# Performance work log

Measured on AMD Instinct MI355X. Metric: run time of the kernel, lower is better.

Reference implementation:

```python
import jax, jax.numpy as jnp
import numpy as np

V = 32000   # vocab_size
H = 256     # num_hiddens
B = 32      # batch
T = 128     # seq_len


def setup_inputs() -> dict:
    key = jax.random.key(0)
    ks = jax.random.split(key, 10)
    s = 0.05  # keep pre-activations in a sane range
    return {
        "X": jax.random.randint(ks[0], (B, T), 0, V),
        "H0": jnp.zeros((B, H), jnp.float32),
        "Wz": (jax.random.normal(ks[1], (H, V + H)) * s).astype(jnp.float32),
        "bz": (jax.random.normal(ks[2], (H,)) * s).astype(jnp.float32),
        "Wr": (jax.random.normal(ks[3], (H, V + H)) * s).astype(jnp.float32),
        "br": (jax.random.normal(ks[4], (H,)) * s).astype(jnp.float32),
        "Wh": (jax.random.normal(ks[5], (H, V + H)) * s).astype(jnp.float32),
        "bh": (jax.random.normal(ks[6], (H,)) * s).astype(jnp.float32),
        "Wo": (jax.random.normal(ks[7], (V, H)) * s).astype(jnp.float32),
        "bo": (jax.random.normal(ks[8], (V,)) * s).astype(jnp.float32),
    }


def reference(X, H0, Wz, bz, Wr, br, Wh, bh, Wo, bo):
    # nn.Linear(cat(one_hot(x), h)) == gather of the vocab-columns + h @ Wh.T.
    # one_hot(x) @ W[:, :V].T  ==  W[:, :V].T[x]  (row gather), same math, no dense one-hot GEMM.
    vocab = Wo.shape[0]
    Wz_x, Wz_h = Wz[:, :vocab], Wz[:, vocab:]
    Wr_x, Wr_h = Wr[:, :vocab], Wr[:, vocab:]
    Wh_x, Wh_h = Wh[:, :vocab], Wh[:, vocab:]

    Xt = X.T                 # [T, B] -- matches X.T in torch forward
    gz = Wz_x.T[Xt]          # [T, B, H]
    gr = Wr_x.T[Xt]          # [T, B, H]
    gh = Wh_x.T[Xt]          # [T, B, H]

    def step(Hs, g):
        gz_t, gr_t, gh_t = g
        z = jax.nn.sigmoid(gz_t + Hs @ Wz_h.T + bz)
        r = jax.nn.sigmoid(gr_t + Hs @ Wr_h.T + br)
        h = jnp.tanh(gh_t + (r * Hs) @ Wh_h.T + bh)
        Hn = z * h + (1.0 - z) * Hs
        Y = Hn @ Wo.T + bo   # [B, V]
        return Hn, Y

    Hf, Ys = jax.lax.scan(step, H0, (gz, gr, gh))  # Ys: [T, B, V]
    # torch.cat(outputs, dim=0) stacks time-major -> [T*B, V]
    return Ys.reshape(-1, vocab), Hf
```

## Files before the change

### kernel.cpp

```cpp
#include <hip/hip_runtime.h>
#include <hip/hip_fp16.h>
#include <stdint.h>

#define VV 32000
#define HH 256
#define BB 32
#define TT 128
#define VH 32256

typedef _Float16 f16;
typedef _Float16 f16x2 __attribute__((ext_vector_type(2)));
typedef _Float16 f16x8 __attribute__((ext_vector_type(8)));
typedef float f32x4 __attribute__((ext_vector_type(4)));

static __device__ __forceinline__ float dot2f(uint32_t w, uint32_t h, float acc){
  f16x2 a = __builtin_bit_cast(f16x2, w);
  f16x2 b = __builtin_bit_cast(f16x2, h);
#if __has_builtin(__builtin_amdgcn_fdot2)
  return __builtin_amdgcn_fdot2(a, b, acc, false);
#else
  acc = fmaf((float)a[0], (float)b[0], acc);
  acc = fmaf((float)a[1], (float)b[1], acc);
  return acc;
#endif
}

__global__ void k_gather(const int* __restrict__ X,
                         const float* __restrict__ Wz, const float* __restrict__ bz,
                         const float* __restrict__ Wr, const float* __restrict__ br,
                         const float* __restrict__ Wh, const float* __restrict__ bh,
                         float* __restrict__ g_buf){
  int tb = blockIdx.x;
  int t = tb >> 5, b = tb & 31;
  int tok = X[b*TT + t];
  int o = threadIdx.x;
  g_buf[(size_t)tb*768 + o]       = Wz[(size_t)o*VH + tok] + bz[o];
  g_buf[(size_t)tb*768 + 256 + o] = Wr[(size_t)o*VH + tok] + br[o];
  g_buf[(size_t)tb*768 + 512 + o] = Wh[(size_t)o*VH + tok] + bh[o];
}

__global__ void k_pack(const float* __restrict__ Wz, const float* __restrict__ Wr,
                       const float* __restrict__ Wh, uint32_t* __restrict__ Wpack){
  int idx = blockIdx.x*256 + threadIdx.x;
  if (idx >= 512*192) return;
  int t = idx / 192, rem = idx - t*192;
  int ol = rem >> 4, p = rem & 15;
  int ko = t & 7, no = t >> 3;
  int k = ko*32 + p*2;
  const float* W; int row;
  if (ol < 8){ int o = no*8 + ol; if (o < 256){ W = Wz; row = o; } else { W = Wr; row = o - 256; } }
  else { W = Wh; row = no*4 + (ol - 8); }
  float a = W[(size_t)row*VH + VV + k];
  float c = W[(size_t)row*VH + VV + k + 1];
  f16x2 v; v[0] = (f16)a; v[1] = (f16)c;
  Wpack[idx] = __builtin_bit_cast(uint32_t, v);
}

__global__ __launch_bounds__(512)
__attribute__((amdgpu_waves_per_eu(2, 2)))
void k_recur(const float* __restrict__ H0,
             const uint32_t* __restrict__ Wpack,
             const float* __restrict__ g_buf,
             f16* __restrict__ Hn16,
             float* __restrict__ hf_out){
  __shared__ __align__(16) uint32_t hs16[128];
  __shared__ __align__(16) f16 rHs16[256];
  __shared__ float hs32[256];
  __shared__ float z_s[256];

  const int b = blockIdx.x;
  const int tid = threadIdx.x;
  const int ko = tid & 7, no = tid >> 3;

  uint32_t w[12][16];
  {
    const uint4* src = (const uint4*)(Wpack + (size_t)tid*192);
    #pragma unroll
    for (int j=0;j<48;j++){
      uint4 v = src[j];
      int f = j*4;
      w[(f+0)>>4][(f+0)&15] = v.x;
      w[(f+1)>>4][(f+1)&15] = v.y;
      w[(f+2)>>4][(f+2)&15] = v.z;
      w[(f+3)>>4][(f+3)&15] = v.w;
    }
  }

  if (tid < 256) hs32[tid] = H0[b*HH + tid];
  __syncthreads();
  if (tid < 128){
    f16x2 v; v[0] = (f16)hs32[2*tid]; v[1] = (f16)hs32[2*tid+1];
    hs16[tid] = __builtin_bit_cast(uint32_t, v);
  }
  __syncthreads();

  const int gi1 = no*8 + ko;
  const int gi2 = 512 + no*4 + (ko & 3);
  float g1 = g_buf[(size_t)b*768 + gi1];
  float g2 = g_buf[(size_t)b*768 + gi2];
  float g1n = 0.f, g2n = 0.f;

  for (int t = 0; t < TT; t++){
    if (t < TT-1){
      const float* gn = g_buf + (size_t)((t+1)*BB + b)*768;
      g1n = gn[gi1];
      g2n = gn[gi2];
    }

    uint32_t hp[16];
    {
      const uint2* hsp = (const uint2*)hs16;
      #pragma unroll
      for (int j=0;j<8;j++){ uint2 v = hsp[ko*8 + j]; hp[2*j] = v.x; hp[2*j+1] = v.y; }
    }
    float acc[8];
    #pragma unroll
    for (int ol=0;ol<8;ol++) acc[ol] = 0.f;
    #pragma unroll
    for (int p=0;p<16;p++)
      #pragma unroll
      for (int ol=0;ol<8;ol++)
        acc[ol] = dot2f(w[ol][p], hp[p], acc[ol]);
    #pragma unroll
    for (int ol=0;ol<8;ol++){
      float v2 = acc[ol];
      v2 += __shfl_xor(v2, 1);
      v2 += __shfl_xor(v2, 2);
      v2 += __shfl_xor(v2, 4);
      acc[ol] = v2;
    }
    {
      float sel = acc[0];
      #pragma unroll
      for (int ol=1;ol<8;ol++) sel = (ko == ol) ? acc[ol] : sel;
      float pre = sel + g1;
      float s = 1.f / (1.f + __expf(-pre));
      int o = no*8 + ko;
      if (no < 32){
        z_s[o] = s;
      } else {
        int op = o - 256;
        rHs16[op] = (f16)(s * hs32[op]);
      }
    }
    __syncthreads();

    uint32_t rp[16];
    {
      const uint2* rpp = (const uint2*)rHs16;
      #pragma unroll
      for (int j=0;j<8;j++){ uint2 v = rpp[ko*8 + j]; rp[2*j] = v.x; rp[2*j+1] = v.y; }
    }
    float a2[4];
    #pragma unroll
    for (int oi=0;oi<4;oi++) a2[oi] = 0.f;
    #pragma unroll
    for (int p=0;p<16;p++)
      #pragma unroll
      for (int oi=0;oi<4;oi++)
        a2[oi] = dot2f(w[8+oi][p], rp[p], a2[oi]);
    #pragma unroll
    for (int oi=0;oi<4;oi++){
      float v2 = a2[oi];
      v2 += __shfl_xor(v2, 1);
      v2 += __shfl_xor(v2, 2);
      v2 += __shfl_xor(v2, 4);
      a2[oi] = v2;
    }
    if (ko < 4){
      float sel = a2[0];
      #pragma unroll
      for (int oi=1;oi<4;oi++) sel = (ko == oi) ? a2[oi] : sel;
      int o = no*4 + ko;
      float pre = sel + g2;
      float ax = fabsf(pre);
      float e = __expf(2.f*ax);
      float th = 1.f - 2.f/(e + 1.f);
      th = copysignf(th, pre);
      float z = z_s[o];
      float hn = z*th + (1.f - z)*hs32[o];
      hs32[o] = hn;
      ((f16*)hs16)[o] = (f16)hn;
      Hn16[(size_t)(t*BB + b)*HH + o] = (f16)hn;
      if (t == TT-1) hf_out[b*HH + o] = hn;
    }
    g1 = g1n; g2 = g2n;
    __syncthreads();
  }
}

__global__ __launch_bounds__(256) void k_gemm(const f16* __restrict__ A, const float* __restrict__ Wo,
                                              const float* __restrict__ bo, float* __restrict__ Y){
  __shared__ __align__(16) f16 a_lds[128*128];
  __shared__ __align__(16) f16 b_lds[128*128];
  const int m0 = blockIdx.x * 128;
  const int n0 = blockIdx.y * 128;
  const int tid = threadIdx.x;
  const int lane = tid & 63, wave = tid >> 6;
  const int wm = wave >> 1, wn = wave & 1;

  f32x4 acc[4][4];
  {
    f32x4 z = {0.f, 0.f, 0.f, 0.f};
    #pragma unroll
    for (int i=0;i<4;i++)
      #pragma unroll
      for (int j=0;j<4;j++) acc[i][j] = z;
  }

  const int srow = tid >> 1, seg = tid & 1;
  #pragma unroll 1
  for (int kt=0; kt<2; kt++){
    const int k0 = kt*128;
    {
      const uint4* asrc = (const uint4*)(A + (size_t)(m0+srow)*256 + k0 + seg*64);
      #pragma unroll
      for (int j=0;j<8;j++){
        uint4 v = asrc[j];
        int byte = (srow*256 + seg*128 + j*16) ^ ((srow&7)<<4);
        *(uint4*)((char*)a_lds + byte) = v;
      }
      const float4* bsrc = (const float4*)(Wo + (size_t)(n0+srow)*256 + k0 + seg*64);
      #pragma unroll
      for (int j=0;j<8;j++){
        float4 f0 = bsrc[2*j], f1 = bsrc[2*j+1];
        f16x8 hv;
        hv[0]=(f16)f0.x; hv[1]=(f16)f0.y; hv[2]=(f16)f0.z; hv[3]=(f16)f0.w;
        hv[4]=(f16)f1.x; hv[5]=(f16)f1.y; hv[6]=(f16)f1.z; hv[7]=(f16)f1.w;
        int byte = (srow*256 + seg*128 + j*16) ^ ((srow&7)<<4);
        *(f16x8*)((char*)b_lds + byte) = hv;
      }
    }
    __syncthreads();
    #pragma unroll
    for (int kk=0; kk<4; kk++){
      const int kbyte = kk*64 + (lane>>4)*16;
      f16x8 af[4], bf[4];
      #pragma unroll
      for (int mi=0;mi<4;mi++){
        int row = wm*64 + mi*16 + (lane&15);
        int byte = (row*256 + kbyte) ^ ((row&7)<<4);
        af[mi] = *(const f16x8*)((const char*)a_lds + byte);
      }
      #pragma unroll
      for (int nj=0;nj<4;nj++){
        int nl = wn*64 + nj*16 + (lane&15);
        int byte = (nl*256 + kbyte) ^ ((nl&7)<<4);
        bf[nj] = *(const f16x8*)((const char*)b_lds + byte);
      }
      #pragma unroll
      for (int mi=0;mi<4;mi++)
        #pragma unroll
        for (int nj=0;nj<4;nj++)
          acc[mi][nj] = __builtin_amdgcn_mfma_f32_16x16x32_f16(af[mi], bf[nj], acc[mi][nj], 0, 0, 0);
    }
    __syncthreads();
  }
  #pragma unroll
  for (int nj=0;nj<4;nj++){
    const int col = n0 + wn*64 + nj*16 + (lane & 15);
    const float bov = bo[col];
    #pragma unroll
    for (int mi=0;mi<4;mi++){
      const int rbase = m0 + wm*64 + mi*16 + (lane>>4)*4;
      #pragma unroll
      for (int r=0;r<4;r++){
        Y[(size_t)(rbase + r)*VV + col] = acc[mi][nj][r] + bov;
      }
    }
  }
}

extern "C" void kernel_launch(void* const* d_in, const int* in_sizes, int n_in,
                              void* d_out, int out_size, void* d_ws, size_t ws_size,
                              hipStream_t stream){
  const int*   X  = (const int*)d_in[0];
  const float* H0 = (const float*)d_in[1];
  const float* Wz = (const float*)d_in[2];
  const float* bz = (const float*)d_in[3];
  const float* Wr = (const float*)d_in[4];
  const float* br = (const float*)d_in[5];
  const float* Wh = (const float*)d_in[6];
  const float* bh = (const float*)d_in[7];
  const float* Wo = (const float*)d_in[8];
  const float* bo = (const float*)d_in[9];
  float* out = (float*)d_out;

  char* ws = (char*)d_ws;
  float*    g_buf = (float*)ws;
  uint32_t* Wpack = (uint32_t*)(ws + 12582912);
  f16*      Hn16  = (f16*)(ws + 12582912 + 393216);

  k_gather<<<4096, 256, 0, stream>>>(X, Wz, bz, Wr, br, Wh, bh, g_buf);
  k_pack<<<384, 256, 0, stream>>>(Wz, Wr, Wh, Wpack);
  k_recur<<<32, 512, 0, stream>>>(H0, Wpack, g_buf, Hn16, out + 131072000LL);
  k_gemm<<<dim3(32, 250), 256, 0, stream>>>(Hn16, Wo, bo, out);
}
```

Baseline: 549.3 us.

## Fuse recurrence and output GEMM into persistent kernel with per-timestep flags

Replaces the separate recurrence and output-projection kernels with one persistent kernel of 256 blocks. The first 32 blocks to claim a role run the GRU recurrence and publish a per-timestep completion counter. The rest pull 128x256 output tiles from an atomic queue, spin-wait until the needed timesteps are done, and stage results through LDS so the store to Y is coalesced. The goal is to overlap the output GEMM and its large Y write with the serial recurrence. The cost is spin-wait and atomic overhead, and correctness depends on recurrence blocks becoming resident first, which the atomic role assignment is meant to guarantee.

```diff
diff --git a/kernel.cpp b/kernel.cpp
--- a/kernel.cpp
+++ b/kernel.cpp
@@ -7,6 +7,7 @@
 #define BB 32
 #define TT 128
 #define VH 32256
+#define NTILE 4000
 
 typedef _Float16 f16;
 typedef _Float16 f16x2 __attribute__((ext_vector_type(2)));
@@ -23,6 +24,11 @@
   acc = fmaf((float)a[1], (float)b[1], acc);
   return acc;
 #endif
+}
+
+__global__ void k_init(int* __restrict__ ctl){
+  int i = blockIdx.x*1024 + threadIdx.x;
+  if (i < 2050) ctl[i] = 0;
 }
 
 __global__ void k_gather(const int* __restrict__ X,
@@ -58,214 +64,247 @@
 
 __global__ __launch_bounds__(512)
 __attribute__((amdgpu_waves_per_eu(2, 2)))
-void k_recur(const float* __restrict__ H0,
-             const uint32_t* __restrict__ Wpack,
-             const float* __restrict__ g_buf,
-             f16* __restrict__ Hn16,
-             float* __restrict__ hf_out){
-  __shared__ __align__(16) uint32_t hs16[128];
-  __shared__ __align__(16) f16 rHs16[256];
-  __shared__ float hs32[256];
-  __shared__ float z_s[256];
-
-  const int b = blockIdx.x;
+void k_fused(const float* __restrict__ H0,
+    const uint32_t* __restrict__ Wpack, const float* __restrict__ g_buf,
+    const float* __restrict__ Wo, const float* __restrict__ bo,
+    f16* __restrict__ Hn16, float* __restrict__ Y, float* __restrict__ hf_out,
+    int* __restrict__ ctl){
+  __shared__ __align__(16) char smem[49152];
+  __shared__ int sh_role;
+  __shared__ int sh_tile;
   const int tid = threadIdx.x;
-  const int ko = tid & 7, no = tid >> 3;
-
-  uint32_t w[12][16];
-  {
-    const uint4* src = (const uint4*)(Wpack + (size_t)tid*192);
-    #pragma unroll
-    for (int j=0;j<48;j++){
-      uint4 v = src[j];
-      int f = j*4;
-      w[(f+0)>>4][(f+0)&15] = v.x;
-      w[(f+1)>>4][(f+1)&15] = v.y;
-      w[(f+2)>>4][(f+2)&15] = v.z;
-      w[(f+3)>>4][(f+3)&15] = v.w;
+  if (tid == 0) sh_role = atomicAdd(&ctl[2048], 1);
+  __syncthreads();
+  const int role = sh_role;
+
+  if (role < BB){
+    const int b = role;
+    uint32_t* hs16  = (uint32_t*)smem;
+    f16*      rHs16 = (f16*)(smem + 512);
+    float*    hs32  = (float*)(smem + 1024);
+    float*    z_s   = (float*)(smem + 2048);
+    const int ko = tid & 7, no = tid >> 3;
+
+    uint32_t w[12][16];
+    {
+      const uint4* src = (const uint4*)(Wpack + (size_t)tid*192);
+      #pragma unroll
+      for (int j=0;j<48;j++){
+        uint4 v = src[j];
+        int f = j*4;
+        w[(f+0)>>4][(f+0)&15] = v.x;
+        w[(f+1)>>4][(f+1)&15] = v.y;
+        w[(f+2)>>4][(f+2)&15] = v.z;
+        w[(f+3)>>4][(f+3)&15] = v.w;
+      }
     }
-  }
-
-  if (tid < 256) hs32[tid] = H0[b*HH + tid];
-  __syncthreads();
-  if (tid < 128){
-    f16x2 v; v[0] = (f16)hs32[2*tid]; v[1] = (f16)hs32[2*tid+1];
-    hs16[tid] = __builtin_bit_cast(uint32_t, v);
-  }
-  __syncthreads();
-
-  const int gi1 = no*8 + ko;
-  const int gi2 = 512 + no*4 + (ko & 3);
-  float g1 = g_buf[(size_t)b*768 + gi1];
-  float g2 = g_buf[(size_t)b*768 + gi2];
-  float g1n = 0.f, g2n = 0.f;
-
-  for (int t = 0; t < TT; t++){
-    if (t < TT-1){
-      const float* gn = g_buf + (size_t)((t+1)*BB + b)*768;
-      g1n = gn[gi1];
-      g2n = gn[gi2];
-    }
-
-    uint32_t hp[16];
-    {
-      const uint2* hsp = (const uint2*)hs16;
-      #pragma unroll
-      for (int j=0;j<8;j++){ uint2 v = hsp[ko*8 + j]; hp[2*j] = v.x; hp[2*j+1] = v.y; }
-    }
-    float acc[8];
-    #pragma unroll
-    for (int ol=0;ol<8;ol++) acc[ol] = 0.f;
-    #pragma unroll
-    for (int p=0;p<16;p++)
-      #pragma unroll
-      for (int ol=0;ol<8;ol++)
-        acc[ol] = dot2f(w[ol][p], hp[p], acc[ol]);
-    #pragma unroll
-    for (int ol=0;ol<8;ol++){
-      float v2 = acc[ol];
-      v2 += __shfl_xor(v2, 1);
-      v2 += __shfl_xor(v2, 2);
-      v2 += __shfl_xor(v2, 4);
-      acc[ol] = v2;
-    }
-    {
-      float sel = acc[0];
-      #pragma unroll
-      for (int ol=1;ol<8;ol++) sel = (ko == ol) ? acc[ol] : sel;
-      float pre = sel + g1;
-      float s = 1.f / (1.f + __expf(-pre));
-      int o = no*8 + ko;
-      if (no < 32){
-        z_s[o] = s;
-      } else {
-        int op = o - 256;
-        rHs16[op] = (f16)(s * hs32[op]);
-      }
+
+    if (tid < 256) hs32[tid] = H0[b*HH + tid];
+    __syncthreads();
+    if (tid < 128){
+      f16x2 v; v[0] = (f16)hs32[2*tid]; v[1] = (f16)hs32[2*tid+1];
+      hs16[tid] = __builtin_bit_cast(uint32_t, v);
     }
     __syncthreads();
 
-    uint32_t rp[16];
-    {
-      const uint2* rpp = (const uint2*)rHs16;
-      #pragma unroll
-      for (int j=0;j<8;j++){ uint2 v = rpp[ko*8 + j]; rp[2*j] = v.x; rp[2*j+1] = v.y; }
+    const int gi1 = no*8 + ko;
+    const int gi2 = 512 + no*4 + (ko & 3);
+    float g1 = g_buf[(size_t)b*768 + gi1];
+    float g2 = g_buf[(size_t)b*768 + gi2];
+    float g1n = 0.f, g2n = 0.f;
+
+    for (int t = 0; t < TT; t++){
+      if (t < TT-1){
+        const float* gn = g_buf + (size_t)((t+1)*BB + b)*768;
+        g1n = gn[gi1];
+        g2n = gn[gi2];
+      }
+
+      uint32_t hp[16];
+      {
+        const uint2* hsp = (const uint2*)hs16;
+        #pragma unroll
+        for (int j=0;j<8;j++){ uint2 v = hsp[ko*8 + j]; hp[2*j] = v.x; hp[2*j+1] = v.y; }
+      }
+      float acc[8];
+      #pragma unroll
+      for (int ol=0;ol<8;ol++) acc[ol] = 0.f;
+      #pragma unroll
+      for (int p=0;p<16;p++)
+        #pragma unroll
+        for (int ol=0;ol<8;ol++)
+          acc[ol] = dot2f(w[ol][p], hp[p], acc[ol]);
+      #pragma unroll
+      for (int ol=0;ol<8;ol++){
+        float v2 = acc[ol];
+        v2 += __shfl_xor(v2, 1);
+        v2 += __shfl_xor(v2, 2);
+        v2 += __shfl_xor(v2, 4);
+        acc[ol] = v2;
+      }
+      {
+        float sel = acc[0];
+        #pragma unroll
+        for (int ol=1;ol<8;ol++) sel = (ko == ol) ? acc[ol] : sel;
+        float pre = sel + g1;
+        float s = 1.f / (1.f + __expf(-pre));
+        int o = no*8 + ko;
+        if (no < 32){
+          z_s[o] = s;
+        } else {
+          int op = o - 256;
+          rHs16[op] = (f16)(s * hs32[op]);
+        }
+      }
+      __syncthreads();
+
+      uint32_t rp[16];
+      {
+        const uint2* rpp = (const uint2*)rHs16;
+        #pragma unroll
+        for (int j=0;j<8;j++){ uint2 v = rpp[ko*8 + j]; rp[2*j] = v.x; rp[2*j+1] = v.y; }
+      }
+      float a2[4];
+      #pragma unroll
+      for (int oi=0;oi<4;oi++) a2[oi] = 0.f;
+      #pragma unroll
+      for (int p=0;p<16;p++)
+        #pragma unroll
+        for (int oi=0;oi<4;oi++)
+          a2[oi] = dot2f(w[8+oi][p], rp[p], a2[oi]);
+      #pragma unroll
+      for (int oi=0;oi<4;oi++){
+        float v2 = a2[oi];
+        v2 += __shfl_xor(v2, 1);
+        v2 += __shfl_xor(v2, 2);
+        v2 += __shfl_xor(v2, 4);
+        a2[oi] = v2;
+      }
+      if (ko < 4){
+        float sel = a2[0];
+        #pragma unroll
+        for (int oi=1;oi<4;oi++) sel = (ko == oi) ? a2[oi] : sel;
+        int o = no*4 + ko;
+        float pre = sel + g2;
+        float ax = fabsf(pre);
+        float e = __expf(2.f*ax);
+        float th = 1.f - 2.f/(e + 1.f);
+        th = copysignf(th, pre);
+        float z = z_s[o];
+        float hn = z*th + (1.f - z)*hs32[o];
+        hs32[o] = hn;
+        ((f16*)hs16)[o] = (f16)hn;
+        Hn16[(size_t)(t*BB + b)*HH + o] = (f16)hn;
+        if (t == TT-1) hf_out[b*HH + o] = hn;
+      }
+      g1 = g1n; g2 = g2n;
+      __syncthreads();
+      if (tid == 0){ __threadfence(); atomicAdd(&ctl[t*16], 1); }
     }
-    float a2[4];
-    #pragma unroll
-    for (int oi=0;oi<4;oi++) a2[oi] = 0.f;
-    #pragma unroll
-    for (int p=0;p<16;p++)
-      #pragma unroll
-      for (int oi=0;oi<4;oi++)
-        a2[oi] = dot2f(w[8+oi][p], rp[p], a2[oi]);
-    #pragma unroll
-    for (int oi=0;oi<4;oi++){
-      float v2 = a2[oi];
-      v2 += __shfl_xor(v2, 1);
-      v2 += __shfl_xor(v2, 2);
-      v2 += __shfl_xor(v2, 4);
-      a2[oi] = v2;
-    }
-    if (ko < 4){
-      float sel = a2[0];
-      #pragma unroll
-      for (int oi=1;oi<4;oi++) sel = (ko == oi) ? a2[oi] : sel;
-      int o = no*4 + ko;
-      float pre = sel + g2;
-      float ax = fabsf(pre);
-      float e = __expf(2.f*ax);
-      float th = 1.f - 2.f/(e + 1.f);
-      th = copysignf(th, pre);
-      float z = z_s[o];
-      float hn = z*th + (1.f - z)*hs32[o];
-      hs32[o] = hn;
-      ((f16*)hs16)[o] = (f16)hn;
-      Hn16[(size_t)(t*BB + b)*HH + o] = (f16)hn;
-      if (t == TT-1) hf_out[b*HH + o] = hn;
-    }
-    g1 = g1n; g2 = g2n;
-    __syncthreads();
-  }
-}
-
-__global__ __launch_bounds__(256) void k_gemm(const f16* __restrict__ A, const float* __restrict__ Wo,
-                                              const float* __restrict__ bo, float* __restrict__ Y){
-  __shared__ __align__(16) f16 a_lds[128*128];
-  __shared__ __align__(16) f16 b_lds[128*128];
-  const int m0 = blockIdx.x * 128;
-  const int n0 = blockIdx.y * 128;
-  const int tid = threadIdx.x;
-  const int lane = tid & 63, wave = tid >> 6;
-  const int wm = wave >> 1, wn = wave & 1;
-
-  f32x4 acc[4][4];
-  {
-    f32x4 z = {0.f, 0.f, 0.f, 0.f};
-    #pragma unroll
-    for (int i=0;i<4;i++)
-      #pragma unroll
-      for (int j=0;j<4;j++) acc[i][j] = z;
-  }
-
-  const int srow = tid >> 1, seg = tid & 1;
-  #pragma unroll 1
-  for (int kt=0; kt<2; kt++){
-    const int k0 = kt*128;
-    {
-      const uint4* asrc = (const uint4*)(A + (size_t)(m0+srow)*256 + k0 + seg*64);
-      #pragma unroll
-      for (int j=0;j<8;j++){
-        uint4 v = asrc[j];
-        int byte = (srow*256 + seg*128 + j*16) ^ ((srow&7)<<4);
-        *(uint4*)((char*)a_lds + byte) = v;
-      }
-      const float4* bsrc = (const float4*)(Wo + (size_t)(n0+srow)*256 + k0 + seg*64);
-      #pragma unroll
-      for (int j=0;j<8;j++){
-        float4 f0 = bsrc[2*j], f1 = bsrc[2*j+1];
-        f16x8 hv;
-        hv[0]=(f16)f0.x; hv[1]=(f16)f0.y; hv[2]=(f16)f0.z; hv[3]=(f16)f0.w;
-        hv[4]=(f16)f1.x; hv[5]=(f16)f1.y; hv[6]=(f16)f1.z; hv[7]=(f16)f1.w;
-        int byte = (srow*256 + seg*128 + j*16) ^ ((srow&7)<<4);
-        *(f16x8*)((char*)b_lds + byte) = hv;
-      }
-    }
-    __syncthreads();
-    #pragma unroll
-    for (int kk=0; kk<4; kk++){
-      const int kbyte = kk*64 + (lane>>4)*16;
-      f16x8 af[4], bf[4];
-      #pragma unroll
-      for (int mi=0;mi<4;mi++){
-        int row = wm*64 + mi*16 + (lane&15);
-        int byte = (row*256 + kbyte) ^ ((row&7)<<4);
-        af[mi] = *(const f16x8*)((const char*)a_lds + byte);
-      }
-      #pragma unroll
-      for (int nj=0;nj<4;nj++){
-        int nl = wn*64 + nj*16 + (lane&15);
-        int byte = (nl*256 + kbyte) ^ ((nl&7)<<4);
-        bf[nj] = *(const f16x8*)((const char*)b_lds + byte);
-      }
-      #pragma unroll
-      for (int mi=0;mi<4;mi++)
-        #pragma unroll
-        for (int nj=0;nj<4;nj++)
-          acc[mi][nj] = __builtin_amdgcn_mfma_f32_16x16x32_f16(af[mi], bf[nj], acc[mi][nj], 0, 0, 0);
-    }
-    __syncthreads();
-  }
-  #pragma unroll
-  for (int nj=0;nj<4;nj++){
-    const int col = n0 + wn*64 + nj*16 + (lane & 15);
-    const float bov = bo[col];
-    #pragma unroll
-    for (int mi=0;mi<4;mi++){
-      const int rbase = m0 + wm*64 + mi*16 + (lane>>4)*4;
-      #pragma unroll
-      for (int r=0;r<4;r++){
-        Y[(size_t)(rbase + r)*VV + col] = acc[mi][nj][r] + bov;
+  } else {
+    char* a_base = smem;
+    char* b_base = smem + 16384;
+    float* lds_ep = (float*)smem;
+    const int lane = tid & 63, wid = tid >> 6;
+    const int wm = wid & 1, wn = wid >> 1;
+    const int arow = tid >> 3, aseg = tid & 7;
+    const int brow = tid >> 1, bseg = tid & 1;
+    int fenced_t = -1;
+    for (;;){
+      if (tid == 0) sh_tile = atomicAdd(&ctl[2049], 1);
+      __syncthreads();
+      const int tile = sh_tile;
+      if (tile >= NTILE) break;
+      const int mg = tile / 125;
+      const int ng = tile - mg*125;
+      const int m0 = mg*128, n0 = ng*256;
+      const int t_need = mg*4 + 3;
+      if (tid == 0 && t_need > fenced_t){
+        while (atomicAdd(&ctl[t_need*16], 0) < BB) __builtin_amdgcn_s_sleep(64);
+        __threadfence();
+        fenced_t = t_need;
+      }
+      __syncthreads();
+
+      f32x4 acc[4][4];
+      {
+        f32x4 z = {0.f,0.f,0.f,0.f};
+        #pragma unroll
+        for (int i=0;i<4;i++)
+          #pragma unroll
+          for (int j=0;j<4;j++) acc[i][j] = z;
+      }
+
+      #pragma unroll 1
+      for (int kt=0; kt<4; kt++){
+        #pragma unroll
+        for (int p=0;p<2;p++){
+          int row = arow + p*64;
+          uint4 av = *(const uint4*)(Hn16 + (size_t)(m0+row)*HH + kt*64 + aseg*8);
+          *(uint4*)(a_base + ((row*128 + aseg*16) ^ ((row&7)<<4))) = av;
+        }
+        {
+          const float4* bs = (const float4*)(Wo + (size_t)(n0+brow)*HH + kt*64 + bseg*32);
+          #pragma unroll
+          for (int j=0;j<4;j++){
+            float4 f0 = bs[2*j], f1 = bs[2*j+1];
+            f16x8 hv;
+            hv[0]=(f16)f0.x; hv[1]=(f16)f0.y; hv[2]=(f16)f0.z; hv[3]=(f16)f0.w;
+            hv[4]=(f16)f1.x; hv[5]=(f16)f1.y; hv[6]=(f16)f1.z; hv[7]=(f16)f1.w;
+            *(f16x8*)(b_base + ((brow*128 + bseg*64 + j*16) ^ ((brow&7)<<4))) = hv;
+          }
+        }
+        __syncthreads();
+        #pragma unroll
+        for (int kk=0; kk<2; kk++){
+          const int kbyte = kk*64 + (lane>>4)*16;
+          f16x8 af[4], bf[4];
+          #pragma unroll
+          for (int mi=0;mi<4;mi++){
+            int row = wm*64 + mi*16 + (lane&15);
+            af[mi] = *(const f16x8*)(a_base + ((row*128 + kbyte) ^ ((row&7)<<4)));
+          }
+          #pragma unroll
+          for (int nj=0;nj<4;nj++){
+            int rb = wn*64 + nj*16 + (lane&15);
+            bf[nj] = *(const f16x8*)(b_base + ((rb*128 + kbyte) ^ ((rb&7)<<4)));
+          }
+          #pragma unroll
+          for (int mi=0;mi<4;mi++)
+            #pragma unroll
+            for (int nj=0;nj<4;nj++)
+              acc[mi][nj] = __builtin_amdgcn_mfma_f32_16x16x32_f16(af[mi], bf[nj], acc[mi][nj], 0, 0, 0);
+        }
+        __syncthreads();
+      }
+
+      const float4 bo4 = *(const float4*)(bo + n0 + lane*4);
+      #pragma unroll 1
+      for (int c=0;c<4;c++){
+        if (wm == (c>>1)){
+          #pragma unroll
+          for (int mi2=0;mi2<2;mi2++){
+            int mi = (c&1)*2 + mi2;
+            #pragma unroll
+            for (int nj=0;nj<4;nj++){
+              int col = wn*64 + nj*16 + (lane&15);
+              #pragma unroll
+              for (int r=0;r<4;r++){
+                int lr = mi2*16 + (lane>>4)*4 + r;
+                lds_ep[lr*260 + col] = acc[mi][nj][r];
+              }
+            }
+          }
+        }
+        __syncthreads();
+        #pragma unroll
+        for (int i=0;i<4;i++){
+          int lr = wid*4 + i;
+          float4 v = *(const float4*)(lds_ep + lr*260 + lane*4);
+          v.x += bo4.x; v.y += bo4.y; v.z += bo4.z; v.w += bo4.w;
+          *(float4*)(Y + (size_t)(m0 + c*32 + lr)*VV + n0 + lane*4) = v;
+        }
+        __syncthreads();
       }
     }
   }
@@ -290,9 +329,10 @@
   float*    g_buf = (float*)ws;
   uint32_t* Wpack = (uint32_t*)(ws + 12582912);
   f16*      Hn16  = (f16*)(ws + 12582912 + 393216);
-
+  int*      ctl   = (int*)(ws + 12582912 + 393216 + 2097152);
+
+  k_init<<<3, 1024, 0, stream>>>(ctl);
   k_gather<<<4096, 256, 0, stream>>>(X, Wz, bz, Wr, br, Wh, bh, g_buf);
   k_pack<<<384, 256, 0, stream>>>(Wz, Wr, Wh, Wpack);
-  k_recur<<<32, 512, 0, stream>>>(H0, Wpack, g_buf, Hn16, out + 131072000LL);
-  k_gemm<<<dim3(32, 250), 256, 0, stream>>>(Hn16, Wo, bo, out);
-}
+  k_fused<<<256, 512, 0, stream>>>(H0, Wpack, g_buf, Wo, bo, Hn16, out, out + 131072000LL, ctl);
+}
```

New measurement: 1.152 ms. +109.7%, slower.

## Halve recurrence block to 256 threads with doubled per-thread register weights

Applied to the files above, without the earlier changes.

The GRU recurrence kernel now runs with 256 threads per batch instead of 512. Each thread holds twice as many packed fp16 weights in registers (384 words), and the pack kernel's layout is reworked to match. Each thread computes 16 gate outputs and 8 candidate outputs per step, with wider LDS loads. The aim is to cut barrier cost and wave count per step, at the price of heavy register pressure (one wave per EU) with possible spilling and less latency hiding.

```diff
diff --git a/kernel.cpp b/kernel.cpp
--- a/kernel.cpp
+++ b/kernel.cpp
@@ -42,22 +42,28 @@
 __global__ void k_pack(const float* __restrict__ Wz, const float* __restrict__ Wr,
                        const float* __restrict__ Wh, uint32_t* __restrict__ Wpack){
   int idx = blockIdx.x*256 + threadIdx.x;
-  if (idx >= 512*192) return;
-  int t = idx / 192, rem = idx - t*192;
-  int ol = rem >> 4, p = rem & 15;
+  if (idx >= 256*384) return;
+  int t = idx / 384, rem = idx - t*384;
   int ko = t & 7, no = t >> 3;
+  const float* W; int row, p;
+  if (rem < 256){
+    int ol = rem >> 4; p = rem & 15;
+    int o = no*16 + ol;
+    if (o < 256){ W = Wz; row = o; } else { W = Wr; row = o - 256; }
+  } else {
+    int rem2 = rem - 256;
+    int ol = rem2 >> 4; p = rem2 & 15;
+    W = Wh; row = no*8 + ol;
+  }
   int k = ko*32 + p*2;
-  const float* W; int row;
-  if (ol < 8){ int o = no*8 + ol; if (o < 256){ W = Wz; row = o; } else { W = Wr; row = o - 256; } }
-  else { W = Wh; row = no*4 + (ol - 8); }
   float a = W[(size_t)row*VH + VV + k];
   float c = W[(size_t)row*VH + VV + k + 1];
   f16x2 v; v[0] = (f16)a; v[1] = (f16)c;
   Wpack[idx] = __builtin_bit_cast(uint32_t, v);
 }
 
-__global__ __launch_bounds__(512)
-__attribute__((amdgpu_waves_per_eu(2, 2)))
+__global__ __launch_bounds__(256)
+__attribute__((amdgpu_waves_per_eu(1, 1)))
 void k_recur(const float* __restrict__ H0,
              const uint32_t* __restrict__ Wpack,
              const float* __restrict__ g_buf,
@@ -72,21 +78,31 @@
   const int tid = threadIdx.x;
   const int ko = tid & 7, no = tid >> 3;
 
-  uint32_t w[12][16];
+  uint32_t w1[16][16];
+  uint32_t w2[8][16];
   {
-    const uint4* src = (const uint4*)(Wpack + (size_t)tid*192);
-    #pragma unroll
-    for (int j=0;j<48;j++){
+    const uint4* src = (const uint4*)(Wpack + (size_t)tid*384);
+    #pragma unroll
+    for (int j=0;j<64;j++){
       uint4 v = src[j];
       int f = j*4;
-      w[(f+0)>>4][(f+0)&15] = v.x;
-      w[(f+1)>>4][(f+1)&15] = v.y;
-      w[(f+2)>>4][(f+2)&15] = v.z;
-      w[(f+3)>>4][(f+3)&15] = v.w;
-    }
-  }
-
-  if (tid < 256) hs32[tid] = H0[b*HH + tid];
+      w1[(f+0)>>4][(f+0)&15] = v.x;
+      w1[(f+1)>>4][(f+1)&15] = v.y;
+      w1[(f+2)>>4][(f+2)&15] = v.z;
+      w1[(f+3)>>4][(f+3)&15] = v.w;
+    }
+    #pragma unroll
+    for (int j=0;j<32;j++){
+      uint4 v = src[64 + j];
+      int f = j*4;
+      w2[(f+0)>>4][(f+0)&15] = v.x;
+      w2[(f+1)>>4][(f+1)&15] = v.y;
+      w2[(f+2)>>4][(f+2)&15] = v.z;
+      w2[(f+3)>>4][(f+3)&15] = v.w;
+    }
+  }
+
+  hs32[tid] = H0[b*HH + tid];
   __syncthreads();
   if (tid < 128){
     f16x2 v; v[0] = (f16)hs32[2*tid]; v[1] = (f16)hs32[2*tid+1];
@@ -94,35 +110,41 @@
   }
   __syncthreads();
 
-  const int gi1 = no*8 + ko;
-  const int gi2 = 512 + no*4 + (ko & 3);
-  float g1 = g_buf[(size_t)b*768 + gi1];
-  float g2 = g_buf[(size_t)b*768 + gi2];
-  float g1n = 0.f, g2n = 0.f;
+  const int gi1a = no*16 + ko;
+  const int gi1b = no*16 + 8 + ko;
+  const int gi2  = 512 + no*8 + ko;
+  float g1a = g_buf[(size_t)b*768 + gi1a];
+  float g1b = g_buf[(size_t)b*768 + gi1b];
+  float g2  = g_buf[(size_t)b*768 + gi2];
+  float g1an = 0.f, g1bn = 0.f, g2n = 0.f;
 
   for (int t = 0; t < TT; t++){
     if (t < TT-1){
       const float* gn = g_buf + (size_t)((t+1)*BB + b)*768;
-      g1n = gn[gi1];
-      g2n = gn[gi2];
+      g1an = gn[gi1a];
+      g1bn = gn[gi1b];
+      g2n  = gn[gi2];
     }
 
     uint32_t hp[16];
     {
-      const uint2* hsp = (const uint2*)hs16;
-      #pragma unroll
-      for (int j=0;j<8;j++){ uint2 v = hsp[ko*8 + j]; hp[2*j] = v.x; hp[2*j+1] = v.y; }
-    }
-    float acc[8];
-    #pragma unroll
-    for (int ol=0;ol<8;ol++) acc[ol] = 0.f;
+      const uint4* hsp = (const uint4*)hs16;
+      #pragma unroll
+      for (int j=0;j<4;j++){
+        uint4 v = hsp[ko*4 + j];
+        hp[4*j] = v.x; hp[4*j+1] = v.y; hp[4*j+2] = v.z; hp[4*j+3] = v.w;
+      }
+    }
+    float acc[16];
+    #pragma unroll
+    for (int ol=0;ol<16;ol++) acc[ol] = 0.f;
     #pragma unroll
     for (int p=0;p<16;p++)
       #pragma unroll
-      for (int ol=0;ol<8;ol++)
-        acc[ol] = dot2f(w[ol][p], hp[p], acc[ol]);
-    #pragma unroll
-    for (int ol=0;ol<8;ol++){
+      for (int ol=0;ol<16;ol++)
+        acc[ol] = dot2f(w1[ol][p], hp[p], acc[ol]);
+    #pragma unroll
+    for (int ol=0;ol<16;ol++){
       float v2 = acc[ol];
       v2 += __shfl_xor(v2, 1);
       v2 += __shfl_xor(v2, 2);
@@ -130,48 +152,59 @@
       acc[ol] = v2;
     }
     {
-      float sel = acc[0];
-      #pragma unroll
-      for (int ol=1;ol<8;ol++) sel = (ko == ol) ? acc[ol] : sel;
-      float pre = sel + g1;
-      float s = 1.f / (1.f + __expf(-pre));
-      int o = no*8 + ko;
-      if (no < 32){
-        z_s[o] = s;
+      float sa = acc[0], sb = acc[8];
+      #pragma unroll
+      for (int ol=1;ol<8;ol++){
+        sa = (ko == ol) ? acc[ol]   : sa;
+        sb = (ko == ol) ? acc[ol+8] : sb;
+      }
+      float prea = sa + g1a;
+      float preb = sb + g1b;
+      float va = 1.f / (1.f + __expf(-prea));
+      float vb = 1.f / (1.f + __expf(-preb));
+      int oa = no*16 + ko;
+      int ob = no*16 + 8 + ko;
+      if (no < 16){
+        z_s[oa] = va;
+        z_s[ob] = vb;
       } else {
-        int op = o - 256;
-        rHs16[op] = (f16)(s * hs32[op]);
+        int opa = oa - 256, opb = ob - 256;
+        rHs16[opa] = (f16)(va * hs32[opa]);
+        rHs16[opb] = (f16)(vb * hs32[opb]);
       }
     }
     __syncthreads();
 
     uint32_t rp[16];
     {
-      const uint2* rpp = (const uint2*)rHs16;
-      #pragma unroll
-      for (int j=0;j<8;j++){ uint2 v = rpp[ko*8 + j]; rp[2*j] = v.x; rp[2*j+1] = v.y; }
-    }
-    float a2[4];
-    #pragma unroll
-    for (int oi=0;oi<4;oi++) a2[oi] = 0.f;
+      const uint4* rpp = (const uint4*)rHs16;
+      #pragma unroll
+      for (int j=0;j<4;j++){
+        uint4 v = rpp[ko*4 + j];
+        rp[4*j] = v.x; rp[4*j+1] = v.y; rp[4*j+2] = v.z; rp[4*j+3] = v.w;
+      }
+    }
+    float a2[8];
+    #pragma unroll
+    for (int oi=0;oi<8;oi++) a2[oi] = 0.f;
     #pragma unroll
     for (int p=0;p<16;p++)
       #pragma unroll
-      for (int oi=0;oi<4;oi++)
-        a2[oi] = dot2f(w[8+oi][p], rp[p], a2[oi]);
-    #pragma unroll
-    for (int oi=0;oi<4;oi++){
+      for (int oi=0;oi<8;oi++)
+        a2[oi] = dot2f(w2[oi][p], rp[p], a2[oi]);
+    #pragma unroll
+    for (int oi=0;oi<8;oi++){
       float v2 = a2[oi];
       v2 += __shfl_xor(v2, 1);
       v2 += __shfl_xor(v2, 2);
       v2 += __shfl_xor(v2, 4);
       a2[oi] = v2;
     }
-    if (ko < 4){
+    {
       float sel = a2[0];
       #pragma unroll
-      for (int oi=1;oi<4;oi++) sel = (ko == oi) ? a2[oi] : sel;
-      int o = no*4 + ko;
+      for (int oi=1;oi<8;oi++) sel = (ko == oi) ? a2[oi] : sel;
+      int o = no*8 + ko;
       float pre = sel + g2;
       float ax = fabsf(pre);
       float e = __expf(2.f*ax);
@@ -184,7 +217,7 @@
       Hn16[(size_t)(t*BB + b)*HH + o] = (f16)hn;
       if (t == TT-1) hf_out[b*HH + o] = hn;
     }
-    g1 = g1n; g2 = g2n;
+    g1a = g1an; g1b = g1bn; g2 = g2n;
     __syncthreads();
   }
 }
@@ -293,6 +326,6 @@
 
   k_gather<<<4096, 256, 0, stream>>>(X, Wz, bz, Wr, br, Wh, bh, g_buf);
   k_pack<<<384, 256, 0, stream>>>(Wz, Wr, Wh, Wpack);
-  k_recur<<<32, 512, 0, stream>>>(H0, Wpack, g_buf, Hn16, out + 131072000LL);
+  k_recur<<<32, 256, 0, stream>>>(H0, Wpack, g_buf, Hn16, out + 131072000LL);
   k_gemm<<<dim3(32, 250), 256, 0, stream>>>(Hn16, Wo, bo, out);
 }
```

Measured after the change: 791.9 us. 44.2% more time.

## Pre-convert Wo to fp16, use 32x32 MFMA and XCD-aware block swizzle in output GEMM

Applied to the files above, without the earlier changes.

Adds a separate kernel that converts Wo to fp16 once per call, so GEMM tiles load half-width data without converting inside the main loop. The output GEMM moves from 16x16x32 to 32x32x16 MFMA with a 2x2 accumulator layout, widens the LDS XOR swizzle to 16 rows, and remaps the 1D grid so consecutive blocks on each XCD share tiles. The goal is less redundant fp32 traffic and conversion work (each Wo tile was re-read and converted by all 32 M-blocks), plus better MFMA throughput and L2 locality. The cost is an extra kernel launch and an extra round trip of Wo through memory.

```diff
diff --git a/kernel.cpp b/kernel.cpp
--- a/kernel.cpp
+++ b/kernel.cpp
@@ -11,7 +11,7 @@
 typedef _Float16 f16;
 typedef _Float16 f16x2 __attribute__((ext_vector_type(2)));
 typedef _Float16 f16x8 __attribute__((ext_vector_type(8)));
-typedef float f32x4 __attribute__((ext_vector_type(4)));
+typedef float f32x16 __attribute__((ext_vector_type(16)));
 
 static __device__ __forceinline__ float dot2f(uint32_t w, uint32_t h, float acc){
   f16x2 a = __builtin_bit_cast(f16x2, w);
@@ -56,6 +56,16 @@
   Wpack[idx] = __builtin_bit_cast(uint32_t, v);
 }
 
+__global__ void k_wo(const float* __restrict__ Wo, f16* __restrict__ Wof){
+  int i = blockIdx.x*256 + threadIdx.x;
+  const float4* s = (const float4*)Wo + (size_t)i*2;
+  float4 f0 = s[0], f1 = s[1];
+  f16x8 h;
+  h[0]=(f16)f0.x; h[1]=(f16)f0.y; h[2]=(f16)f0.z; h[3]=(f16)f0.w;
+  h[4]=(f16)f1.x; h[5]=(f16)f1.y; h[6]=(f16)f1.z; h[7]=(f16)f1.w;
+  *(f16x8*)(Wof + (size_t)i*8) = h;
+}
+
 __global__ __launch_bounds__(512)
 __attribute__((amdgpu_waves_per_eu(2, 2)))
 void k_recur(const float* __restrict__ H0,
@@ -189,23 +199,24 @@
   }
 }
 
-__global__ __launch_bounds__(256) void k_gemm(const f16* __restrict__ A, const float* __restrict__ Wo,
+__global__ __launch_bounds__(256) void k_gemm(const f16* __restrict__ A, const f16* __restrict__ Wof,
                                               const float* __restrict__ bo, float* __restrict__ Y){
   __shared__ __align__(16) f16 a_lds[128*128];
   __shared__ __align__(16) f16 b_lds[128*128];
-  const int m0 = blockIdx.x * 128;
-  const int n0 = blockIdx.y * 128;
+  const int wg = (blockIdx.x & 7)*1000 + (blockIdx.x >> 3);
+  const int m0 = (wg & 31) * 128;
+  const int n0 = (wg >> 5) * 128;
   const int tid = threadIdx.x;
   const int lane = tid & 63, wave = tid >> 6;
   const int wm = wave >> 1, wn = wave & 1;
 
-  f32x4 acc[4][4];
+  f32x16 acc[2][2];
   {
-    f32x4 z = {0.f, 0.f, 0.f, 0.f};
-    #pragma unroll
-    for (int i=0;i<4;i++)
-      #pragma unroll
-      for (int j=0;j<4;j++) acc[i][j] = z;
+    f32x16 z = {0.f};
+    #pragma unroll
+    for (int i=0;i<2;i++)
+      #pragma unroll
+      for (int j=0;j<2;j++) acc[i][j] = z;
   }
 
   const int srow = tid >> 1, seg = tid & 1;
@@ -214,58 +225,52 @@
     const int k0 = kt*128;
     {
       const uint4* asrc = (const uint4*)(A + (size_t)(m0+srow)*256 + k0 + seg*64);
+      const uint4* bsrc = (const uint4*)(Wof + (size_t)(n0+srow)*256 + k0 + seg*64);
       #pragma unroll
       for (int j=0;j<8;j++){
-        uint4 v = asrc[j];
-        int byte = (srow*256 + seg*128 + j*16) ^ ((srow&7)<<4);
-        *(uint4*)((char*)a_lds + byte) = v;
-      }
-      const float4* bsrc = (const float4*)(Wo + (size_t)(n0+srow)*256 + k0 + seg*64);
-      #pragma unroll
-      for (int j=0;j<8;j++){
-        float4 f0 = bsrc[2*j], f1 = bsrc[2*j+1];
-        f16x8 hv;
-        hv[0]=(f16)f0.x; hv[1]=(f16)f0.y; hv[2]=(f16)f0.z; hv[3]=(f16)f0.w;
-        hv[4]=(f16)f1.x; hv[5]=(f16)f1.y; hv[6]=(f16)f1.z; hv[7]=(f16)f1.w;
-        int byte = (srow*256 + seg*128 + j*16) ^ ((srow&7)<<4);
-        *(f16x8*)((char*)b_lds + byte) = hv;
+        uint4 av = asrc[j];
+        int byte = (srow*256 + ((seg*128 + j*16) ^ ((srow&15)<<4)));
+        *(uint4*)((char*)a_lds + byte) = av;
+        uint4 bv = bsrc[j];
+        *(uint4*)((char*)b_lds + byte) = bv;
       }
     }
     __syncthreads();
     #pragma unroll
-    for (int kk=0; kk<4; kk++){
-      const int kbyte = kk*64 + (lane>>4)*16;
-      f16x8 af[4], bf[4];
-      #pragma unroll
-      for (int mi=0;mi<4;mi++){
-        int row = wm*64 + mi*16 + (lane&15);
-        int byte = (row*256 + kbyte) ^ ((row&7)<<4);
+    for (int kk=0; kk<8; kk++){
+      const int kbyte = kk*32 + (lane>>5)*16;
+      f16x8 af[2], bf[2];
+      #pragma unroll
+      for (int mi=0;mi<2;mi++){
+        int row = wm*64 + mi*32 + (lane&31);
+        int byte = (row*256 + (kbyte ^ ((row&15)<<4)));
         af[mi] = *(const f16x8*)((const char*)a_lds + byte);
       }
       #pragma unroll
-      for (int nj=0;nj<4;nj++){
-        int nl = wn*64 + nj*16 + (lane&15);
-        int byte = (nl*256 + kbyte) ^ ((nl&7)<<4);
+      for (int nj=0;nj<2;nj++){
+        int nl = wn*64 + nj*32 + (lane&31);
+        int byte = (nl*256 + (kbyte ^ ((nl&15)<<4)));
         bf[nj] = *(const f16x8*)((const char*)b_lds + byte);
       }
       #pragma unroll
-      for (int mi=0;mi<4;mi++)
+      for (int mi=0;mi<2;mi++)
         #pragma unroll
-        for (int nj=0;nj<4;nj++)
-          acc[mi][nj] = __builtin_amdgcn_mfma_f32_16x16x32_f16(af[mi], bf[nj], acc[mi][nj], 0, 0, 0);
+        for (int nj=0;nj<2;nj++)
+          acc[mi][nj] = __builtin_amdgcn_mfma_f32_32x32x16_f16(af[mi], bf[nj], acc[mi][nj], 0, 0, 0);
     }
     __syncthreads();
   }
   #pragma unroll
-  for (int nj=0;nj<4;nj++){
-    const int col = n0 + wn*64 + nj*16 + (lane & 15);
+  for (int nj=0;nj<2;nj++){
+    const int col = n0 + wn*64 + nj*32 + (lane & 31);
     const float bov = bo[col];
     #pragma unroll
-    for (int mi=0;mi<4;mi++){
-      const int rbase = m0 + wm*64 + mi*16 + (lane>>4)*4;
-      #pragma unroll
-      for (int r=0;r<4;r++){
-        Y[(size_t)(rbase + r)*VV + col] = acc[mi][nj][r] + bov;
+    for (int mi=0;mi<2;mi++){
+      const int rbase = m0 + wm*64 + mi*32 + 4*(lane>>5);
+      #pragma unroll
+      for (int r=0;r<16;r++){
+        int row = rbase + (r&3) + 8*(r>>2);
+        Y[(size_t)row*VV + col] = acc[mi][nj][r] + bov;
       }
     }
   }
@@ -290,9 +295,11 @@
   float*    g_buf = (float*)ws;
   uint32_t* Wpack = (uint32_t*)(ws + 12582912);
   f16*      Hn16  = (f16*)(ws + 12582912 + 393216);
+  f16*      Wof   = (f16*)(ws + 12582912 + 393216 + 2097152);
 
   k_gather<<<4096, 256, 0, stream>>>(X, Wz, bz, Wr, br, Wh, bh, g_buf);
   k_pack<<<384, 256, 0, stream>>>(Wz, Wr, Wh, Wpack);
+  k_wo<<<4000, 256, 0, stream>>>(Wo, Wof);
   k_recur<<<32, 512, 0, stream>>>(H0, Wpack, g_buf, Hn16, out + 131072000LL);
-  k_gemm<<<dim3(32, 250), 256, 0, stream>>>(Hn16, Wo, bo, out);
-}
+  k_gemm<<<8000, 256, 0, stream>>>(Hn16, Wof, bo, out);
+}
```

After: 527.8 us. 3.9% less time.
